# Performance work log

Measured on AMD Instinct MI355X. Metric: run time of the kernel, lower is better.

Reference implementation:

```python
import jax, jax.numpy as jnp
import numpy as np

EMBED_DIM = 2048
NUM_HEADS = 16
HEAD_DIM = EMBED_DIM // NUM_HEADS
BATCH = 4
SEQ = 1024
ROPE_BASE = 10000.0


def _rotate_half(x):
    x1, x2 = jnp.split(x, 2, axis=-1)
    return jnp.concatenate([-x2, x1], axis=-1)


def setup_inputs() -> dict:
    key = jax.random.key(0)
    ks = jax.random.split(key, 8)
    query = jax.random.normal(ks[0], (BATCH, SEQ, EMBED_DIM), dtype=jnp.float32)
    kkey = jax.random.normal(ks[1], (BATCH, SEQ, EMBED_DIM), dtype=jnp.float32)
    value = jax.random.normal(ks[2], (BATCH, SEQ, EMBED_DIM), dtype=jnp.float32)
    # causal mask: scores.masked_fill(mask == 0, -inf)
    mask = jnp.tril(jnp.ones((SEQ, SEQ), dtype=jnp.int32))[None, None]
    # RoPE tables [S, head_dim]
    inv_freq = 1.0 / (ROPE_BASE ** (np.arange(0, HEAD_DIM, 2, dtype=np.float32) / HEAD_DIM))
    pos = np.arange(SEQ, dtype=np.float32)
    freqs = np.outer(pos, inv_freq)                      # [S, D/2]
    emb = np.concatenate([freqs, freqs], axis=-1)        # [S, D]
    rope_cos = jnp.asarray(np.cos(emb), dtype=jnp.float32)
    rope_sin = jnp.asarray(np.sin(emb), dtype=jnp.float32)
    s = 1.0 / np.sqrt(EMBED_DIM)
    Wq = jax.random.normal(ks[3], (EMBED_DIM, EMBED_DIM), dtype=jnp.float32) * s
    Wk = jax.random.normal(ks[4], (EMBED_DIM, EMBED_DIM), dtype=jnp.float32) * s
    Wv = jax.random.normal(ks[5], (EMBED_DIM, EMBED_DIM), dtype=jnp.float32) * s
    Wo = jax.random.normal(ks[6], (EMBED_DIM, EMBED_DIM), dtype=jnp.float32) * s
    return {"query": query, "key": kkey, "value": value, "mask": mask,
            "rope_cos": rope_cos, "rope_sin": rope_sin,
            "Wq": Wq, "Wk": Wk, "Wv": Wv, "Wo": Wo}


def reference(query, key, value, mask, rope_cos, rope_sin, Wq, Wk, Wv, Wo):
    B, S, E = query.shape
    # projections (nn.Linear: x @ W.T)
    def proj(x, W):
        y = x @ W.T
        return y.reshape(B, -1, NUM_HEADS, HEAD_DIM).transpose(0, 2, 1, 3)  # [B,H,S,D]
    Q = proj(query, Wq)
    K = proj(key, Wk)
    V = proj(value, Wv)
    # RoPE (rotate-half form), cos/sin broadcast over batch and heads
    cos = rope_cos[None, None]  # [1,1,S,D]
    sin = rope_sin[None, None]
    Q = Q * cos + _rotate_half(Q) * sin
    K = K * cos + _rotate_half(K) * sin
    scale = jnp.asarray(np.sqrt(HEAD_DIM), dtype=Q.dtype)
    scores = jnp.einsum('bhqd,bhkd->bhqk', Q, K) / scale
    scores = jnp.where(mask == 0, jnp.asarray(-jnp.inf, scores.dtype), scores)
    attn = jax.nn.softmax(scores, axis=-1)
    context = jnp.einsum('bhqk,bhkd->bhqd', attn, V)
    context = context.transpose(0, 2, 1, 3).reshape(B, S, E)
    out = context @ Wo.T
    return out
```

## Files before the change

kernel.cpp:

```cpp
#include <hip/hip_runtime.h>
#include <stdint.h>

#define E_DIM 2048
#define N_HEADS 16
#define H_DIM 128
#define BATCH 4
#define SEQL 1024
#define M_ROWS 4096

typedef __attribute__((ext_vector_type(8))) short bf16x8;
typedef __attribute__((ext_vector_type(4))) float f32x4;

#define AS1 __attribute__((address_space(1)))
#define AS3 __attribute__((address_space(3)))

__device__ __forceinline__ void gload16(const void* g, void* l) {
  __builtin_amdgcn_global_load_lds((const AS1 uint32_t*)g, (AS3 uint32_t*)l, 16, 0, 0);
}

__device__ __forceinline__ unsigned short f2bf(float f) {
  union { float f; uint32_t u; } v; v.f = f;
  return (unsigned short)((v.u + 0x7FFFu + ((v.u >> 16) & 1u)) >> 16);
}

__global__ __launch_bounds__(256) void k_cvt(
    const float* __restrict__ q, const float* __restrict__ k, const float* __restrict__ v,
    const float* __restrict__ wq, const float* __restrict__ wk,
    const float* __restrict__ wv, const float* __restrict__ wo,
    ushort* __restrict__ oq, ushort* __restrict__ ok, ushort* __restrict__ ov,
    ushort* __restrict__ owq, ushort* __restrict__ owk,
    ushort* __restrict__ owv, ushort* __restrict__ owo) {
  int y = blockIdx.y;
  const float* in;
  ushort* out;
  if (y < 3) {
    in = (y == 0) ? q : (y == 1) ? k : v;
    out = (y == 0) ? oq : (y == 1) ? ok : ov;
  } else {
    if (blockIdx.x >= 4096) return;
    in = (y == 3) ? wq : (y == 4) ? wk : (y == 5) ? wv : wo;
    out = (y == 3) ? owq : (y == 4) ? owk : (y == 5) ? owv : owo;
  }
  int i = (blockIdx.x * 256 + threadIdx.x) * 4;
  float4 vv = *reinterpret_cast<const float4*>(in + i);
  *reinterpret_cast<ushort4*>(out + i) =
      make_ushort4(f2bf(vv.x), f2bf(vv.y), f2bf(vv.z), f2bf(vv.w));
}

template <int NREP>
__device__ __forceinline__ void gemm256_mainloop(const ushort* __restrict__ A,
                                                 const ushort* __restrict__ W,
                                                 ushort* lds, int m0, int n0,
                                                 const int browRows[NREP],
                                                 f32x4 (&acc)[8][NREP]) {
  const int tid = threadIdx.x;
  const int w = tid >> 6, lane = tid & 63, quad = lane >> 4, lid = lane & 15;
  constexpr int BELE = NREP * 4096;
  ushort* bufA[2] = {lds, lds + 16384};
  ushort* bufB[2] = {lds + 32768, lds + 32768 + BELE};

  const int p0 = tid, p1i = tid + 512;
  const int r0 = p0 >> 3, c0 = (p0 & 7) ^ (r0 & 7);
  const int r1 = p1i >> 3, c1 = (p1i & 7) ^ (r1 & 7);
  const int ld0 = (w * 64) * 8;
  const int ld1 = (512 + w * 64) * 8;

  const ushort* gA = A + (size_t)m0 * E_DIM;
  const ushort* gB = W + (size_t)n0 * E_DIM;

  auto stage = [&](const ushort* g, ushort* buf, int kt, int half) {
    const ushort* s0p = g + (size_t)(half * 128 + r0) * E_DIM + kt * 64 + c0 * 8;
    const ushort* s1p = g + (size_t)(half * 128 + r1) * E_DIM + kt * 64 + c1 * 8;
    ushort* l = buf + half * 8192;
    gload16(s0p, l + ld0);
    gload16(s1p, l + ld1);
  };

  int ofsA[2], ofsB[NREP][2];
  {
    const int rowA = (w >> 2) * 128 + lid;
#pragma unroll
    for (int ks = 0; ks < 2; ++ks)
      ofsA[ks] = rowA * 64 + (((ks * 4 + quad) ^ (lid & 7)) * 8);
#pragma unroll
    for (int ni = 0; ni < NREP; ++ni)
#pragma unroll
      for (int ks = 0; ks < 2; ++ks)
        ofsB[ni][ks] = browRows[ni] * 64 + (((ks * 4 + quad) ^ (lid & 7)) * 8);
  }

  bf16x8 bfr[NREP][2];

#define VMW_N                                                                  \
  do {                                                                         \
    if constexpr (NREP == 4)                                                   \
      asm volatile("s_waitcnt vmcnt(4)" ::: "memory");                         \
    else                                                                       \
      asm volatile("s_waitcnt vmcnt(2)" ::: "memory");                         \
  } while (0)

#define PH(b, q, STGS, VMW)                                                    \
  do {                                                                         \
    bf16x8 af[2][2];                                                           \
    if ((q) == 0) {                                                            \
      _Pragma("unroll") for (int ni = 0; ni < NREP; ++ni)                      \
          _Pragma("unroll") for (int ks = 0; ks < 2; ++ks)                     \
              bfr[ni][ks] =                                                    \
                  *reinterpret_cast<const bf16x8*>(bufB[b] + ofsB[ni][ks]);    \
    }                                                                          \
    _Pragma("unroll") for (int d = 0; d < 2; ++d)                              \
        _Pragma("unroll") for (int ks = 0; ks < 2; ++ks)                       \
            af[d][ks] = *reinterpret_cast<const bf16x8*>(                      \
                bufA[b] + ofsA[ks] + ((q) * 2 + d) * 1024);                    \
    STGS;                                                                      \
    VMW;                                                                       \
    __builtin_amdgcn_s_barrier();                                              \
    asm volatile("s_waitcnt lgkmcnt(0)" ::: "memory");                         \
    __builtin_amdgcn_s_setprio(1);                                             \
    _Pragma("unroll") for (int ks = 0; ks < 2; ++ks)                           \
        _Pragma("unroll") for (int d = 0; d < 2; ++d)                          \
            _Pragma("unroll") for (int ni = 0; ni < NREP; ++ni)                \
                acc[(q) * 2 + d][ni] = __builtin_amdgcn_mfma_f32_16x16x32_bf16(\
                    af[d][ks], bfr[ni][ks], acc[(q) * 2 + d][ni], 0, 0, 0);    \
    __builtin_amdgcn_s_setprio(0);                                             \
    __builtin_amdgcn_s_barrier();                                              \
  } while (0)

  stage(gB, bufB[0], 0, 0); if (NREP == 4) stage(gB, bufB[0], 0, 1);
  stage(gA, bufA[0], 0, 0); stage(gA, bufA[0], 0, 1);
  stage(gB, bufB[1], 1, 0); if (NREP == 4) stage(gB, bufB[1], 1, 1);
  VMW_N;
  __builtin_amdgcn_s_barrier();

  for (int i = 0; i < 16; ++i) {
    const bool lastI = (i == 15);
    const int tn = 2 * i;
    PH(0, 0, stage(gA, bufA[1], tn + 1, 0), );
    PH(0, 1, stage(gA, bufA[1], tn + 1, 1), );
    PH(0, 2, if (!lastI) stage(gB, bufB[0], tn + 2, 0), );
    PH(0, 3, if (!lastI && NREP == 4) stage(gB, bufB[0], tn + 2, 1),
       if (lastI) asm volatile("s_waitcnt vmcnt(0)" ::: "memory");
       else VMW_N);
    PH(1, 0, if (!lastI) stage(gA, bufA[0], tn + 2, 0), );
    PH(1, 1, if (!lastI) stage(gA, bufA[0], tn + 2, 1), );
    PH(1, 2, if (!lastI) stage(gB, bufB[1], tn + 3, 0), );
    PH(1, 3, if (!lastI && NREP == 4) stage(gB, bufB[1], tn + 3, 1),
       if (!lastI) VMW_N);
  }
#undef PH
#undef VMW_N
}

__global__ __launch_bounds__(512, 2) void k_gemm_qkv(
    const ushort* __restrict__ xq, const ushort* __restrict__ xk, const ushort* __restrict__ xv,
    const ushort* __restrict__ wq, const ushort* __restrict__ wk, const ushort* __restrict__ wv,
    ushort* __restrict__ Qr, ushort* __restrict__ Kr, ushort* __restrict__ Vr,
    const float* __restrict__ cosT, const float* __restrict__ sinT) {
  extern __shared__ ushort lds[];
  const int z = blockIdx.z;
  const ushort* A = (z == 0) ? xq : (z == 1) ? xk : xv;
  const ushort* W = (z == 0) ? wq : (z == 1) ? wk : wv;
  ushort* Out = (z == 0) ? Qr : (z == 1) ? Kr : Vr;
  const int tid = threadIdx.x;
  const int w = tid >> 6, lane = tid & 63, quad = lane >> 4, lid = lane & 15;
  const int wn = w & 3;
  const int n0 = blockIdx.x * 256;
  const int m0 = blockIdx.y * 256;

  int browRows[4];
#pragma unroll
  for (int ni = 0; ni < 4; ++ni)
    browRows[ni] = (wn >> 1) * 128 + (wn & 1) * 32 + (ni & 1) * 16 + (ni >> 1) * 64 + lid;

  f32x4 acc[8][4];
  const f32x4 z4 = {0.f, 0.f, 0.f, 0.f};
#pragma unroll
  for (int i = 0; i < 8; ++i)
#pragma unroll
    for (int j = 0; j < 4; ++j) acc[i][j] = z4;

  gemm256_mainloop<4>(A, W, lds, m0, n0, browRows, acc);

  const int b = m0 >> 10;
  const int h = blockIdx.x * 2 + (wn >> 1);
  ushort* Og = Out + (size_t)(b * N_HEADS + h) * SEQL * H_DIM;
  const bool rope = (z < 2);
#pragma unroll
  for (int mi = 0; mi < 8; ++mi)
#pragma unroll
    for (int r = 0; r < 4; ++r) {
      int s = (m0 & (SEQL - 1)) + (w >> 2) * 128 + mi * 16 + quad * 4 + r;
      size_t row = (size_t)s * H_DIM;
      if (rope) {
#pragma unroll
        for (int ni = 0; ni < 2; ++ni) {
          int d0 = (wn & 1) * 32 + ni * 16 + lid;
          float c = cosT[s * H_DIM + d0];
          float sn = sinT[s * H_DIM + d0];
          float x0 = acc[mi][ni][r], x1 = acc[mi][ni + 2][r];
          Og[row + d0]      = f2bf(x0 * c - x1 * sn);
          Og[row + d0 + 64] = f2bf(x1 * c + x0 * sn);
        }
      } else {
#pragma unroll
        for (int ni = 0; ni < 4; ++ni) {
          int d = (wn & 1) * 32 + (ni & 1) * 16 + (ni >> 1) * 64 + lid;
          Og[row + d] = f2bf(acc[mi][ni][r]);
        }
      }
    }
}

__global__ __launch_bounds__(512, 2) void k_gemm_o(const ushort* __restrict__ A,
                                                   const ushort* __restrict__ W,
                                                   float* __restrict__ Out) {
  extern __shared__ ushort lds[];
  const int tid = threadIdx.x;
  const int w = tid >> 6, lane = tid & 63, quad = lane >> 4, lid = lane & 15;
  const int wn = w & 3;
  const int n0 = blockIdx.x * 128;
  const int m0 = blockIdx.y * 256;

  int browRows[2];
#pragma unroll
  for (int ni = 0; ni < 2; ++ni) browRows[ni] = wn * 32 + ni * 16 + lid;

  f32x4 acc[8][2];
  const f32x4 z4 = {0.f, 0.f, 0.f, 0.f};
#pragma unroll
  for (int i = 0; i < 8; ++i)
#pragma unroll
    for (int j = 0; j < 2; ++j) acc[i][j] = z4;

  gemm256_mainloop<2>(A, W, lds, m0, n0, browRows, acc);

#pragma unroll
  for (int mi = 0; mi < 8; ++mi)
#pragma unroll
    for (int r = 0; r < 4; ++r) {
      size_t row = (size_t)(m0 + (w >> 2) * 128 + mi * 16 + quad * 4 + r) * E_DIM + n0;
#pragma unroll
      for (int ni = 0; ni < 2; ++ni) Out[row + browRows[ni]] = acc[mi][ni][r];
    }
}

__global__ __launch_bounds__(256) void k_transv(const ushort* __restrict__ V,
                                                ushort* __restrict__ Vt) {
  __shared__ ushort t[32][33];
  int bh = blockIdx.z;
  int s0 = blockIdx.x * 32;
  int d0 = blockIdx.y * 32;
  int j = threadIdx.x & 31;
  int i = threadIdx.x >> 5;
  for (int rr = 0; rr < 4; ++rr) {
    int row = i + rr * 8;
    t[row][j] = V[((size_t)bh * SEQL + s0 + row) * H_DIM + d0 + j];
  }
  __syncthreads();
  for (int rr = 0; rr < 4; ++rr) {
    int drow = i + rr * 8;
    Vt[((size_t)bh * H_DIM + d0 + drow) * SEQL + s0 + j] = t[j][drow];
  }
}

__global__ __launch_bounds__(256, 2) void k_attn(const ushort* __restrict__ Q,
                                                 const ushort* __restrict__ K,
                                                 const ushort* __restrict__ Vt,
                                                 ushort* __restrict__ Ctx) {
  extern __shared__ ushort lds[];
  const int tid = threadIdx.x;
  const int w = tid >> 6, lane = tid & 63, quad = lane >> 4, lid = lane & 15;
  ushort* Pw = lds + 32768 + w * 1280;

  const int l = blockIdx.y * 8 + blockIdx.x;
  const int bh = l & 63;
  const int slot = l >> 6;
  const int qt = (slot < 4) ? slot : 11 - slot;
  const int q0 = qt * 128;
  const size_t base = (size_t)bh * SEQL * H_DIM;
  const ushort* Qg = Q + base;
  const ushort* Kg = K + base;
  const ushort* Vg = Vt + base;

  auto stageK = [&](ushort* dst, int j0) {
#pragma unroll
    for (int i = 0; i < 4; ++i) {
      int g = i * 256 + tid;
      int kk = g >> 4;
      int c = (g & 15) ^ (kk & 15);
      gload16(Kg + (size_t)(j0 + kk) * H_DIM + c * 8, dst + (i * 256 + w * 64) * 8);
    }
  };
  auto stageV = [&](ushort* dst, int j0) {
#pragma unroll
    for (int i = 0; i < 4; ++i) {
      int g = i * 256 + tid;
      int d = g >> 3;
      int c = (g & 7) ^ (d & 7);
      gload16(Vg + (size_t)d * SEQL + j0 + c * 8, dst + (i * 256 + w * 64) * 8);
    }
  };

  bf16x8 qf[2][4];
  for (int mt = 0; mt < 2; ++mt) {
    int row = q0 + w * 32 + mt * 16 + lid;
    for (int kc = 0; kc < 4; ++kc)
      qf[mt][kc] = *reinterpret_cast<const bf16x8*>(Qg + (size_t)row * H_DIM + kc * 32 + quad * 8);
  }

  f32x4 oacc[2][8];
  f32x4 lacc[2];
  const f32x4 z4 = {0.f, 0.f, 0.f, 0.f};
  for (int mt = 0; mt < 2; ++mt) {
    lacc[mt] = z4;
    for (int dt = 0; dt < 8; ++dt) oacc[mt][dt] = z4;
  }

  bf16x8 ones;
  for (int i = 0; i < 8; ++i) ones[i] = (short)0x3F80;

  const float SC2 = 0.08838834764831845f * 1.4426950408889634f;
  const float M2 = 12.0f * 1.4426950408889634f;

  ushort *Kc = lds, *Kn = lds + 8192;
  ushort *Vc = lds + 16384, *Vn = lds + 24576;

  const int NT = (q0 >> 6) + 2;
  stageK(Kc, 0);
  stageV(Vc, 0);
  __syncthreads();

  for (int t = 0; t < NT; ++t) {
    const int j0 = t << 6;
    if (t + 1 < NT) { stageK(Kn, j0 + 64); stageV(Vn, j0 + 64); }

    f32x4 sacc[2][4];
    for (int mt = 0; mt < 2; ++mt)
      for (int nt = 0; nt < 4; ++nt) sacc[mt][nt] = z4;
    __builtin_amdgcn_s_setprio(1);
    for (int kc = 0; kc < 4; ++kc)
      for (int nt = 0; nt < 4; ++nt) {
        int kk = nt * 16 + lid;
        bf16x8 kf = *reinterpret_cast<const bf16x8*>(
            Kc + kk * H_DIM + (((kc * 4 + quad) ^ lid) * 8));
        sacc[0][nt] = __builtin_amdgcn_mfma_f32_16x16x32_bf16(qf[0][kc], kf, sacc[0][nt], 0, 0, 0);
        sacc[1][nt] = __builtin_amdgcn_mfma_f32_16x16x32_bf16(qf[1][kc], kf, sacc[1][nt], 0, 0, 0);
      }
    __builtin_amdgcn_s_setprio(0);

    if (j0 + 64 > q0) {
      for (int mt = 0; mt < 2; ++mt)
        for (int nt = 0; nt < 4; ++nt)
          for (int r = 0; r < 4; ++r) {
            int key = j0 + nt * 16 + lid;
            int row = q0 + w * 32 + mt * 16 + quad * 4 + r;
            if (key > row) sacc[mt][nt][r] = -3.0e38f;
          }
    }

    for (int h4 = 0; h4 < 2; ++h4) {
      for (int mt = 0; mt < 2; ++mt)
        for (int half = 0; half < 2; ++half) {
          int nt = h4 * 2 + half;
          for (int r = 0; r < 4; ++r) {
            float p = exp2f(fmaf(sacc[mt][nt][r], SC2, -M2));
            Pw[(mt * 16 + quad * 4 + r) * 40 + half * 16 + lid] = f2bf(p);
          }
        }
      bf16x8 pf0 = *reinterpret_cast<const bf16x8*>(Pw + lid * 40 + quad * 8);
      bf16x8 pf1 = *reinterpret_cast<const bf16x8*>(Pw + (16 + lid) * 40 + quad * 8);
      lacc[0] = __builtin_amdgcn_mfma_f32_16x16x32_bf16(pf0, ones, lacc[0], 0, 0, 0);
      lacc[1] = __builtin_amdgcn_mfma_f32_16x16x32_bf16(pf1, ones, lacc[1], 0, 0, 0);
      __builtin_amdgcn_s_setprio(1);
      for (int dt = 0; dt < 8; ++dt) {
        int d = dt * 16 + lid;
        bf16x8 vf = *reinterpret_cast<const bf16x8*>(
            Vc + d * 64 + (((h4 * 4 + quad) ^ (d & 7)) * 8));
        oacc[0][dt] = __builtin_amdgcn_mfma_f32_16x16x32_bf16(pf0, vf, oacc[0][dt], 0, 0, 0);
        oacc[1][dt] = __builtin_amdgcn_mfma_f32_16x16x32_bf16(pf1, vf, oacc[1][dt], 0, 0, 0);
      }
      __builtin_amdgcn_s_setprio(0);
    }

    __syncthreads();
    ushort* t0 = Kc; Kc = Kn; Kn = t0;
    ushort* t1 = Vc; Vc = Vn; Vn = t1;
  }

  const int b = bh >> 4, h = bh & 15;
  for (int mt = 0; mt < 2; ++mt)
    for (int r = 0; r < 4; ++r) {
      int s = q0 + w * 32 + mt * 16 + quad * 4 + r;
      float inv = 1.0f / lacc[mt][r];
      for (int dt = 0; dt < 8; ++dt)
        Ctx[(size_t)(b * SEQL + s) * E_DIM + h * H_DIM + dt * 16 + lid] =
            f2bf(oacc[mt][dt][r] * inv);
    }
}

extern "C" void kernel_launch(void* const* d_in, const int* in_sizes, int n_in,
                              void* d_out, int out_size, void* d_ws, size_t ws_size,
                              hipStream_t stream) {
  const float* q_in = (const float*)d_in[0];
  const float* k_in = (const float*)d_in[1];
  const float* v_in = (const float*)d_in[2];
  const float* rc = (const float*)d_in[4];
  const float* rs = (const float*)d_in[5];
  const float* Wq = (const float*)d_in[6];
  const float* Wk = (const float*)d_in[7];
  const float* Wv = (const float*)d_in[8];
  const float* Wo = (const float*)d_in[9];
  float* out = (float*)d_out;

  ushort* p = (ushort*)d_ws;
  const size_t WSZ = (size_t)E_DIM * E_DIM;
  const size_t XSZ = (size_t)M_ROWS * E_DIM;
  ushort* wq_b = p; p += WSZ;
  ushort* wk_b = p; p += WSZ;
  ushort* wv_b = p; p += WSZ;
  ushort* wo_b = p; p += WSZ;
  ushort* xq_b = p; p += XSZ;
  ushort* xk_b = p; p += XSZ;
  ushort* xv_b = p; p += XSZ;
  ushort* Qr = p;   p += XSZ;
  ushort* Kr = p;   p += XSZ;
  ushort* Vr = p;   p += XSZ;
  ushort* Vt = p;   p += XSZ;
  ushort* ctx = xq_b;

  (void)hipFuncSetAttribute(reinterpret_cast<const void*>(k_gemm_qkv),
                            hipFuncAttributeMaxDynamicSharedMemorySize, 131072);
  (void)hipFuncSetAttribute(reinterpret_cast<const void*>(k_gemm_o),
                            hipFuncAttributeMaxDynamicSharedMemorySize, 98304);
  (void)hipFuncSetAttribute(reinterpret_cast<const void*>(k_attn),
                            hipFuncAttributeMaxDynamicSharedMemorySize, 75776);

  dim3 blk(256);
  k_cvt<<<dim3(8192, 7), blk, 0, stream>>>(q_in, k_in, v_in, Wq, Wk, Wv, Wo,
                                           xq_b, xk_b, xv_b, wq_b, wk_b, wv_b, wo_b);

  k_gemm_qkv<<<dim3(E_DIM / 256, M_ROWS / 256, 3), dim3(512), 131072, stream>>>(
      xq_b, xk_b, xv_b, wq_b, wk_b, wv_b, Qr, Kr, Vr, rc, rs);

  k_transv<<<dim3(SEQL / 32, H_DIM / 32, BATCH * N_HEADS), blk, 0, stream>>>(Vr, Vt);

  k_attn<<<dim3(8, BATCH * N_HEADS), blk, 75776, stream>>>(Qr, Kr, Vt, ctx);

  k_gemm_o<<<dim3(E_DIM / 128, M_ROWS / 256), dim3(512), 98304, stream>>>(ctx, wo_b, out);
}
```

Measured before the change: 394.8 us.

## Fuse V transpose into QKV GEMM epilogue and remap attention block schedule

The V projection epilogue now stages the bf16 tile through LDS and writes V directly in transposed [d][s] layout. This removes the separate k_transv kernel and its extra global round trip of V. Dynamic LDS for the QKV GEMM grows to 135168 bytes to hold the padded transpose tile, which could affect occupancy. The attention kernel's block-to-(bh, q-tile) mapping is also changed to pair long and short causal tiles differently for load balance.

```diff
diff --git a/kernel.cpp b/kernel.cpp
--- a/kernel.cpp
+++ b/kernel.cpp
@@ -154,13 +154,12 @@
 __global__ __launch_bounds__(512, 2) void k_gemm_qkv(
     const ushort* __restrict__ xq, const ushort* __restrict__ xk, const ushort* __restrict__ xv,
     const ushort* __restrict__ wq, const ushort* __restrict__ wk, const ushort* __restrict__ wv,
-    ushort* __restrict__ Qr, ushort* __restrict__ Kr, ushort* __restrict__ Vr,
+    ushort* __restrict__ Qr, ushort* __restrict__ Kr, ushort* __restrict__ Vt,
     const float* __restrict__ cosT, const float* __restrict__ sinT) {
   extern __shared__ ushort lds[];
   const int z = blockIdx.z;
   const ushort* A = (z == 0) ? xq : (z == 1) ? xk : xv;
   const ushort* W = (z == 0) ? wq : (z == 1) ? wk : wv;
-  ushort* Out = (z == 0) ? Qr : (z == 1) ? Kr : Vr;
   const int tid = threadIdx.x;
   const int w = tid >> 6, lane = tid & 63, quad = lane >> 4, lid = lane & 15;
   const int wn = w & 3;
@@ -182,16 +181,16 @@
   gemm256_mainloop<4>(A, W, lds, m0, n0, browRows, acc);
 
   const int b = m0 >> 10;
-  const int h = blockIdx.x * 2 + (wn >> 1);
-  ushort* Og = Out + (size_t)(b * N_HEADS + h) * SEQL * H_DIM;
-  const bool rope = (z < 2);
-#pragma unroll
-  for (int mi = 0; mi < 8; ++mi)
-#pragma unroll
-    for (int r = 0; r < 4; ++r) {
-      int s = (m0 & (SEQL - 1)) + (w >> 2) * 128 + mi * 16 + quad * 4 + r;
-      size_t row = (size_t)s * H_DIM;
-      if (rope) {
+  if (z < 2) {
+    ushort* Out = (z == 0) ? Qr : Kr;
+    const int h = blockIdx.x * 2 + (wn >> 1);
+    ushort* Og = Out + (size_t)(b * N_HEADS + h) * SEQL * H_DIM;
+#pragma unroll
+    for (int mi = 0; mi < 8; ++mi)
+#pragma unroll
+      for (int r = 0; r < 4; ++r) {
+        int s = (m0 & (SEQL - 1)) + (w >> 2) * 128 + mi * 16 + quad * 4 + r;
+        size_t row = (size_t)s * H_DIM;
 #pragma unroll
         for (int ni = 0; ni < 2; ++ni) {
           int d0 = (wn & 1) * 32 + ni * 16 + lid;
@@ -201,14 +200,34 @@
           Og[row + d0]      = f2bf(x0 * c - x1 * sn);
           Og[row + d0 + 64] = f2bf(x1 * c + x0 * sn);
         }
-      } else {
-#pragma unroll
-        for (int ni = 0; ni < 4; ++ni) {
-          int d = (wn & 1) * 32 + (ni & 1) * 16 + (ni >> 1) * 64 + lid;
-          Og[row + d] = f2bf(acc[mi][ni][r]);
-        }
       }
-    }
+  } else {
+    __syncthreads();
+    ushort* T = lds;
+    const int sl0 = (w >> 2) * 128 + quad * 4;
+#pragma unroll
+    for (int mi = 0; mi < 8; ++mi)
+#pragma unroll
+      for (int ni = 0; ni < 4; ++ni) {
+        ushort4 pk;
+        pk.x = f2bf(acc[mi][ni][0]);
+        pk.y = f2bf(acc[mi][ni][1]);
+        pk.z = f2bf(acc[mi][ni][2]);
+        pk.w = f2bf(acc[mi][ni][3]);
+        *reinterpret_cast<ushort4*>(T + browRows[ni] * 264 + sl0 + mi * 16) = pk;
+      }
+    __syncthreads();
+    const int sg = (m0 & (SEQL - 1));
+#pragma unroll
+    for (int r32 = 0; r32 < 32; ++r32) {
+      int c = w * 32 + r32;
+      int d = c & 127;
+      int h = blockIdx.x * 2 + (c >> 7);
+      ushort4 v4 = *reinterpret_cast<const ushort4*>(T + c * 264 + lane * 4);
+      *reinterpret_cast<ushort4*>(
+          Vt + ((size_t)((b * N_HEADS + h) * H_DIM + d)) * SEQL + sg + lane * 4) = v4;
+    }
+  }
 }
 
 __global__ __launch_bounds__(512, 2) void k_gemm_o(const ushort* __restrict__ A,
@@ -244,25 +263,6 @@
     }
 }
 
-__global__ __launch_bounds__(256) void k_transv(const ushort* __restrict__ V,
-                                                ushort* __restrict__ Vt) {
-  __shared__ ushort t[32][33];
-  int bh = blockIdx.z;
-  int s0 = blockIdx.x * 32;
-  int d0 = blockIdx.y * 32;
-  int j = threadIdx.x & 31;
-  int i = threadIdx.x >> 5;
-  for (int rr = 0; rr < 4; ++rr) {
-    int row = i + rr * 8;
-    t[row][j] = V[((size_t)bh * SEQL + s0 + row) * H_DIM + d0 + j];
-  }
-  __syncthreads();
-  for (int rr = 0; rr < 4; ++rr) {
-    int drow = i + rr * 8;
-    Vt[((size_t)bh * H_DIM + d0 + drow) * SEQL + s0 + j] = t[j][drow];
-  }
-}
-
 __global__ __launch_bounds__(256, 2) void k_attn(const ushort* __restrict__ Q,
                                                  const ushort* __restrict__ K,
                                                  const ushort* __restrict__ Vt,
@@ -273,30 +273,31 @@
   ushort* Pw = lds + 32768 + w * 1280;
 
   const int l = blockIdx.y * 8 + blockIdx.x;
-  const int bh = l & 63;
-  const int slot = l >> 6;
-  const int qt = (slot < 4) ? slot : 11 - slot;
+  const int g = (l & 1) ^ ((l >> 8) & 1);
+  const int base = (l >> 1) & 7;
+  const int qt = g ? 7 - base : base;
+  const int bh = ((l >> 4) & 31) | (g << 5);
   const int q0 = qt * 128;
-  const size_t base = (size_t)bh * SEQL * H_DIM;
-  const ushort* Qg = Q + base;
-  const ushort* Kg = K + base;
-  const ushort* Vg = Vt + base;
+  const size_t bse = (size_t)bh * SEQL * H_DIM;
+  const ushort* Qg = Q + bse;
+  const ushort* Kg = K + bse;
+  const ushort* Vg = Vt + bse;
 
   auto stageK = [&](ushort* dst, int j0) {
 #pragma unroll
     for (int i = 0; i < 4; ++i) {
-      int g = i * 256 + tid;
-      int kk = g >> 4;
-      int c = (g & 15) ^ (kk & 15);
+      int g2 = i * 256 + tid;
+      int kk = g2 >> 4;
+      int c = (g2 & 15) ^ (kk & 15);
       gload16(Kg + (size_t)(j0 + kk) * H_DIM + c * 8, dst + (i * 256 + w * 64) * 8);
     }
   };
   auto stageV = [&](ushort* dst, int j0) {
 #pragma unroll
     for (int i = 0; i < 4; ++i) {
-      int g = i * 256 + tid;
-      int d = g >> 3;
-      int c = (g & 7) ^ (d & 7);
+      int g2 = i * 256 + tid;
+      int d = g2 >> 3;
+      int c = (g2 & 7) ^ (d & 7);
       gload16(Vg + (size_t)d * SEQL + j0 + c * 8, dst + (i * 256 + w * 64) * 8);
     }
   };
@@ -424,12 +425,11 @@
   ushort* xv_b = p; p += XSZ;
   ushort* Qr = p;   p += XSZ;
   ushort* Kr = p;   p += XSZ;
-  ushort* Vr = p;   p += XSZ;
   ushort* Vt = p;   p += XSZ;
   ushort* ctx = xq_b;
 
   (void)hipFuncSetAttribute(reinterpret_cast<const void*>(k_gemm_qkv),
-                            hipFuncAttributeMaxDynamicSharedMemorySize, 131072);
+                            hipFuncAttributeMaxDynamicSharedMemorySize, 135168);
   (void)hipFuncSetAttribute(reinterpret_cast<const void*>(k_gemm_o),
                             hipFuncAttributeMaxDynamicSharedMemorySize, 98304);
   (void)hipFuncSetAttribute(reinterpret_cast<const void*>(k_attn),
@@ -439,10 +439,8 @@
   k_cvt<<<dim3(8192, 7), blk, 0, stream>>>(q_in, k_in, v_in, Wq, Wk, Wv, Wo,
                                            xq_b, xk_b, xv_b, wq_b, wk_b, wv_b, wo_b);
 
-  k_gemm_qkv<<<dim3(E_DIM / 256, M_ROWS / 256, 3), dim3(512), 131072, stream>>>(
-      xq_b, xk_b, xv_b, wq_b, wk_b, wv_b, Qr, Kr, Vr, rc, rs);
-
-  k_transv<<<dim3(SEQL / 32, H_DIM / 32, BATCH * N_HEADS), blk, 0, stream>>>(Vr, Vt);
+  k_gemm_qkv<<<dim3(E_DIM / 256, M_ROWS / 256, 3), dim3(512), 135168, stream>>>(
+      xq_b, xk_b, xv_b, wq_b, wk_b, wv_b, Qr, Kr, Vt, rc, rs);
 
   k_attn<<<dim3(8, BATCH * N_HEADS), blk, 75776, stream>>>(Qr, Kr, Vt, ctx);
 
```

New measurement: 385.3 us. 2.4% less time.
